# Kernel optimization log

Hardware: AMD Instinct MI355X
Metric: run time of the kernel (lower is better)

The kernel has to match this reference:

```python
import jax, jax.numpy as jnp
from jax import lax
import numpy as np

B, CIN, T, H, W = 32, 512, 16, 7, 7
A = 9                 # 3 scales x 3 ratios
STRIDE = 16.0
NMS_THRESH = 0.7      # cfg.TEST.RPN_NMS_THRESH
POST_NMS = 300        # cfg.TEST.RPN_POST_NMS_TOP_N


def _gen_anchors():
    # faithful port of generate_anchors(base_size=16, ratios=[0.5,1,2], scales=[4,8,16])
    base = 16.0
    ratios = np.array([0.5, 1.0, 2.0])
    scales = np.array([4.0, 8.0, 16.0])
    ctr = (base - 1.0) / 2.0
    size = base * base
    ws = np.round(np.sqrt(size / ratios))
    hs = np.round(ws * ratios)
    def mk(ws, hs, xc, yc):
        return np.stack([xc - 0.5 * (ws - 1), yc - 0.5 * (hs - 1),
                         xc + 0.5 * (ws - 1), yc + 0.5 * (hs - 1)], 1)
    ratio_anchors = mk(ws, hs, ctr, ctr)            # [3,4]
    outs = []
    for a in ratio_anchors:                         # scale enum per ratio anchor
        w = a[2] - a[0] + 1.0
        h = a[3] - a[1] + 1.0
        xc = a[0] + 0.5 * (w - 1)
        yc = a[1] + 0.5 * (h - 1)
        outs.append(mk(w * scales, h * scales, xc, yc))
    return np.concatenate(outs, 0).astype(np.float32)  # [9,4]


def _shifted_anchors():
    sx = (np.arange(W) * STRIDE).astype(np.float32)
    sy = (np.arange(H) * STRIDE).astype(np.float32)
    mx, my = np.meshgrid(sx, sy)                    # x fastest, matches HWA flatten
    shifts = np.stack([mx.ravel(), my.ravel(), mx.ravel(), my.ravel()], 1)  # [K,4]
    return (shifts[:, None, :] + _gen_anchors()[None, :, :]).reshape(-1, 4)  # [K*A,4]

_ALL_ANCHORS = jnp.asarray(_shifted_anchors())      # [441,4]


def conv3d(x, w, b, pad):
    y = lax.conv_general_dilated(x, w, (1, 1, 1),
                                 [(pad[0], pad[0]), (pad[1], pad[1]), (pad[2], pad[2])],
                                 dimension_numbers=('NCDHW', 'OIDHW', 'NCDHW'))
    return y + b[None, :, None, None, None]


def conv1x1(x, w, b):
    return jnp.einsum('bchw,oc->bohw', x, w[:, :, 0, 0]) + b[None, :, None, None]


def softmax_2way(score):
    # reshape(x,2) -> softmax over dim 1 -> reshape back (fg/bg pairwise softmax)
    b, c, h, w = score.shape
    s = score.reshape(b, 2, (c // 2) * h, w)
    return jax.nn.softmax(s, axis=1).reshape(b, c, h, w)


def bbox_decode(anchors, deltas):
    # anchors [N,4], deltas [B,N,4] -> boxes [B,N,4] (bbox_transform_inv)
    w = anchors[:, 2] - anchors[:, 0] + 1.0
    h = anchors[:, 3] - anchors[:, 1] + 1.0
    cx = anchors[:, 0] + 0.5 * w
    cy = anchors[:, 1] + 0.5 * h
    pcx = deltas[..., 0] * w + cx
    pcy = deltas[..., 1] * h + cy
    pw = jnp.exp(deltas[..., 2]) * w
    ph = jnp.exp(deltas[..., 3]) * h
    return jnp.stack([pcx - 0.5 * pw, pcy - 0.5 * ph,
                      pcx + 0.5 * pw, pcy + 0.5 * ph], axis=-1)


def clip_boxes(boxes, info):
    # boxes [N,4], info = (im_h, im_w, scale)
    x1 = jnp.clip(boxes[:, 0], 0.0, info[1] - 1.0)
    y1 = jnp.clip(boxes[:, 1], 0.0, info[0] - 1.0)
    x2 = jnp.clip(boxes[:, 2], 0.0, info[1] - 1.0)
    y2 = jnp.clip(boxes[:, 3], 0.0, info[0] - 1.0)
    return jnp.stack([x1, y1, x2, y2], 1)


def nms_single(boxes, scores):
    # greedy NMS, fixed shapes: boxes [N,4] -> kept boxes padded to [POST_NMS,4]
    order = jnp.argsort(-scores)
    b = boxes[order]
    n = b.shape[0]
    areas = (b[:, 2] - b[:, 0] + 1.0) * (b[:, 3] - b[:, 1] + 1.0)
    idx = jnp.arange(n)
    def body(i, keep):
        xx1 = jnp.maximum(b[i, 0], b[:, 0])
        yy1 = jnp.maximum(b[i, 1], b[:, 1])
        xx2 = jnp.minimum(b[i, 2], b[:, 2])
        yy2 = jnp.minimum(b[i, 3], b[:, 3])
        inter = jnp.clip(xx2 - xx1 + 1.0, 0.0) * jnp.clip(yy2 - yy1 + 1.0, 0.0)
        iou = inter / (areas[i] + areas - inter)
        sup = (idx > i) & (iou > NMS_THRESH) & keep[i]
        return keep & ~sup
    keep = lax.fori_loop(0, n, body, jnp.ones((n,), bool))
    sel = jnp.sort(jnp.where(keep, idx, n))[:POST_NMS]
    valid = sel < n
    selc = jnp.minimum(sel, n - 1)
    return jnp.where(valid[:, None], b[selc], 0.0)


def proposal_layer(cls_prob, bbox_pred, im_info):
    b = cls_prob.shape[0]
    scores = cls_prob[:, A:, :, :].transpose(0, 2, 3, 1).reshape(b, -1)   # fg scores [B,K*A]
    deltas = bbox_pred.transpose(0, 2, 3, 1).reshape(b, -1, 4)
    props = bbox_decode(_ALL_ANCHORS, deltas)
    props = jax.vmap(clip_boxes)(props, im_info)
    boxes = jax.vmap(nms_single)(props, scores)                           # [B,POST_NMS,4]
    bidx = jnp.broadcast_to(jnp.arange(b, dtype=boxes.dtype)[:, None, None],
                            (b, POST_NMS, 1))
    return jnp.concatenate([bidx, boxes], axis=2)                         # [B,POST_NMS,5]


def setup_inputs() -> dict:
    key = jax.random.key(0)
    ks = jax.random.split(key, 8)
    s = 0.05
    return {
        'base_feat': jax.random.normal(ks[0], (B, CIN, T, H, W), jnp.float32),
        'im_info': jnp.tile(jnp.array([[112.0, 112.0, 1.0]], jnp.float32), (B, 1)),
        'gt_boxes': jnp.zeros((B, 1, 7), jnp.float32),
        'num_boxes': jnp.zeros((B,), jnp.int32),
        'rpn_conv_w': jax.random.normal(ks[1], (512, CIN, 3, 3, 3), jnp.float32) * s,
        'rpn_conv_b': jnp.zeros((512,), jnp.float32),
        't16_w': jax.random.normal(ks[2], (512, 512, 16, 3, 3), jnp.float32) * s,
        't16_b': jnp.zeros((512,), jnp.float32),
        'cls_w': jax.random.normal(ks[3], (2 * A, 512, 1, 1), jnp.float32) * s,
        'cls_b': jnp.zeros((2 * A,), jnp.float32),
        'bbox_w': jax.random.normal(ks[4], (4 * A, 512, 1, 1), jnp.float32) * s,
        'bbox_b': jnp.zeros((4 * A,), jnp.float32),
    }


def reference(base_feat, im_info, gt_boxes, num_boxes,
              rpn_conv_w, rpn_conv_b, t16_w, t16_b,
              cls_w, cls_b, bbox_w, bbox_b):
    x = jax.nn.relu(conv3d(base_feat, rpn_conv_w, rpn_conv_b, (1, 1, 1)))     # [B,512,16,7,7]
    f16 = jax.nn.relu(conv3d(x, t16_w, t16_b, (0, 1, 1)))                     # [B,512,1,7,7]
    f16 = f16.transpose(0, 2, 1, 3, 4).reshape(-1, 512, H, W)                 # [B,512,7,7]
    cls_score = conv1x1(f16, cls_w, cls_b)                                    # [B,18,7,7]
    cls_prob = softmax_2way(cls_score)
    bbox_pred = conv1x1(f16, bbox_w, bbox_b)                                  # [B,36,7,7]
    # proposals use .data in the original -> detached
    rois = proposal_layer(lax.stop_gradient(cls_prob),
                          lax.stop_gradient(bbox_pred), im_info)
    return rois, cls_prob, bbox_pred
```

## Files before the change

kernel.cpp:

```cpp
#include <hip/hip_runtime.h>
#include <hip/hip_bf16.h>
#include <cmath>

typedef __bf16 bf16_t;
typedef unsigned short u16;
typedef unsigned int u32;
typedef float f32x4 __attribute__((ext_vector_type(4)));
typedef short s16x8 __attribute__((ext_vector_type(8)));
typedef u32   u32x4 __attribute__((ext_vector_type(4)));
#define DEVINL __device__ __forceinline__
#define POSTN 300

#define XPT_OFF  0ull
#define YT_OFF   23887872ull
#define F_OFF    45121536ull
#define PART_OFF 48332800ull
#define SC_OFF   51544064ull
#define BX_OFF   51600512ull
#define K1_OFF   51826304ull
#define K2_OFF   51881600ull
#define FLAG_OFF 52176512ull
#define NEED     52176516ull

DEVINL float ldf(const void* p, long i, int f32m) {
  return f32m ? ((const float*)p)[i] : (float)(((const bf16_t*)p)[i]);
}

DEVINL float clampf(float v, float lo, float hi) {
  if (!(v == v)) return lo;
  if (v < lo) return lo;
  if (v > hi) return hi;
  return v;
}

DEVINL u16 b16u(float v) {
  bf16_t h = (bf16_t)v;
  u16 r;
  __builtin_memcpy(&r, &h, 2);
  return r;
}

__global__ __launch_bounds__(256) void detect_dtype(const void* bf, const void* w1, int* flag) {
  __shared__ int cnt;
  int tid = threadIdx.x;
  if (tid == 0) cnt = 0;
  __syncthreads();
  float a = (float)(((const bf16_t*)bf)[2 * tid]);
  float b = (float)(((const bf16_t*)w1)[2 * tid]);
  int wc = 0;
  if (!(a == a) || fabsf(a) > 1e20f || (a != 0.f && fabsf(a) < 1e-20f)) wc++;
  if (!(b == b) || fabsf(b) > 1e20f || (b != 0.f && fabsf(b) < 1e-20f)) wc++;
  atomicAdd(&cnt, wc);
  __syncthreads();
  if (tid == 0) *flag = (cnt >= 16) ? 1 : 0;
}

__global__ __launch_bounds__(256) void build_koff(int* k1, int* k2) {
  int i = blockIdx.x * 256 + threadIdx.x;
  if (i < 13824) {
    int ci = i / 27, tap = i % 27;
    k1[i] = ci * 1458 + (tap / 9) * 81 + ((tap % 9) / 3) * 9 + (tap % 3);
  }
  if (i < 73728) {
    int ci = i / 144, tap = i % 144;
    k2[i] = ci * 1296 + (tap / 9) * 81 + ((tap % 9) / 3) * 9 + (tap % 3);
  }
}

__global__ __launch_bounds__(256) void pad_x(const void* __restrict__ X, float* __restrict__ XpT,
                                             const int* __restrict__ flagp, int cb) {
  int f32m = *flagp;
  long e = (long)blockIdx.x * 256 + threadIdx.x;
  if (e >= 8L * 512 * 784) return;
  int f = (int)(e % 784);
  long bc = e / 784;
  int t = f / 49, h = (f % 49) / 7, w = f % 7;
  float v = ldf(X, ((long)cb * 512 * 784) + bc * 784 + f, f32m);
  XpT[bc * 1458 + (t + 1) * 81 + (h + 1) * 9 + (w + 1)] = v;
}

template <int MODE>
__global__ __launch_bounds__(256) void gemm_f32(
    const float* __restrict__ Act, const void* __restrict__ Wgt, const void* __restrict__ bias,
    float* __restrict__ Yt, float* __restrict__ Part,
    const int* __restrict__ koff, const int* __restrict__ flagp) {
  const int f32m = *flagp;
  if (MODE == 1 && f32m == 0) return;
  const int tid = threadIdx.x;
  int mt, nt, s = 0;
  if (MODE == 1) { mt = blockIdx.x % 98; nt = blockIdx.x / 98; }
  else           { mt = blockIdx.x % 7;  nt = (blockIdx.x / 7) % 8; s = blockIdx.x / 56; }
  const int m0 = mt * 64, n0 = nt * 64;
  const int K     = (MODE == 1) ? 13824 : 18432;
  const int kBase = (MODE == 1) ? 0     : s * 18432;
  const int WROW  = (MODE == 1) ? 13824 : 73728;

  __shared__ __align__(16) float As[64][68];
  __shared__ __align__(16) float Bs[64][68];

  const int am = tid & 63, akq = tid >> 6;
  long aBase;
  {
    int m = m0 + am;
    if (MODE == 1) {
      int b = m / 784, r = m % 784, t = r / 49, h = (r % 49) / 7, w = r % 7;
      aBase = (long)b * (512 * 1458) + t * 81 + h * 9 + w;
    } else {
      if (m > 391) m = 391;
      int b = m / 49, r = m % 49, h = r / 7, w = r % 7;
      aBase = (long)b * (512 * 1296) + h * 9 + w;
    }
  }
  const int bn = tid >> 2, bks = (tid & 3) * 16;
  const long bBase = (long)(n0 + bn) * WROW + kBase;

  float acc[4][4] = {{0.f}};
  const int tx = tid & 15, ty = tid >> 4;

  for (int k0 = 0; k0 < K; k0 += 64) {
    __syncthreads();
#pragma unroll
    for (int j = 0; j < 16; j++) {
      int kk = akq * 16 + j;
      As[kk][am] = Act[aBase + koff[kBase + k0 + kk]];
    }
#pragma unroll
    for (int j = 0; j < 16; j++) {
      int kk = bks + j;
      Bs[kk][bn] = ldf(Wgt, bBase + k0 + kk, f32m);
    }
    __syncthreads();
#pragma unroll 8
    for (int k = 0; k < 64; k++) {
      f32x4 a = *(const f32x4*)&As[k][tx * 4];
      f32x4 b = *(const f32x4*)&Bs[k][ty * 4];
#pragma unroll
      for (int i = 0; i < 4; i++)
#pragma unroll
        for (int j = 0; j < 4; j++) acc[i][j] += a[i] * b[j];
    }
  }

#pragma unroll
  for (int i = 0; i < 4; i++) {
    int m = m0 + tx * 4 + i;
#pragma unroll
    for (int j = 0; j < 4; j++) {
      int n = n0 + ty * 4 + j;
      if (MODE == 1) {
        int b = m / 784, r = m % 784, t = r / 49, h = (r % 49) / 7, w = r % 7;
        float v = acc[i][j] + ldf(bias, n, f32m);
        v = fmaxf(v, 0.f);
        Yt[(long)(b * 512 + n) * 1296 + t * 81 + (h + 1) * 9 + (w + 1)] = v;
      } else {
        if (m < 392) Part[((long)s * 392 + m) * 512 + n] = acc[i][j];
      }
    }
  }
}

__global__ __launch_bounds__(256) void gemm_mf1(
    const float* __restrict__ Act, const void* __restrict__ Wgt, const void* __restrict__ bias,
    float* __restrict__ Yt, const int* __restrict__ koff, const int* __restrict__ flagp) {
  if (*flagp != 0) return;
  const int tid = threadIdx.x;
  const int mt = blockIdx.x % 49, nt = blockIdx.x / 49;
  const int m0 = mt * 128, n0 = nt * 64;

  __shared__ u16 As[128 * 64];
  __shared__ u16 Bs[64 * 64];

  const int am = tid & 127, khu = tid >> 7;
  long aBase;
  {
    int m = m0 + am;
    int b = m / 784, r = m % 784, t = r / 49, h = (r % 49) / 7, w = r % 7;
    aBase = (long)b * (512 * 1458) + t * 81 + h * 9 + w;
  }
  const float* __restrict__ Ap = Act + aBase;
  const int awb = am * 64, asw = (am & 7) << 3;

  const int bn = tid & 63, bq = tid >> 6;
  const u16* __restrict__ Bp = (const u16*)Wgt + (long)(n0 + bn) * 13824;
  const int bwb = bn * 64, bsw = (bn & 7) << 3;

  const int lane = tid & 63, wv = tid >> 6;
  const int wm = (wv & 1) * 64, wn = (wv >> 1) * 32;
  const int lr = lane & 15, lq = lane >> 4;

  f32x4 acc[4][2];
#pragma unroll
  for (int i = 0; i < 4; ++i)
#pragma unroll
    for (int j = 0; j < 2; ++j) acc[i][j] = f32x4{0.f, 0.f, 0.f, 0.f};

  for (int k0 = 0; k0 < 13824; k0 += 64) {
    __syncthreads();
#pragma unroll
    for (int j = 0; j < 4; ++j) {
      const int o = k0 + khu * 32 + j * 8;
      const u16 e0 = b16u(Ap[koff[o + 0]]), e1 = b16u(Ap[koff[o + 1]]);
      const u16 e2 = b16u(Ap[koff[o + 2]]), e3 = b16u(Ap[koff[o + 3]]);
      const u16 e4 = b16u(Ap[koff[o + 4]]), e5 = b16u(Ap[koff[o + 5]]);
      const u16 e6 = b16u(Ap[koff[o + 6]]), e7 = b16u(Ap[koff[o + 7]]);
      u32x4 V = { (u32)e0 | ((u32)e1 << 16), (u32)e2 | ((u32)e3 << 16),
                  (u32)e4 | ((u32)e5 << 16), (u32)e6 | ((u32)e7 << 16) };
      *(u32x4*)&As[awb + ((khu * 32 + j * 8) ^ asw)] = V;
    }
    {
      const u32x4* wp = (const u32x4*)(Bp + k0 + bq * 16);
      *(u32x4*)&Bs[bwb + ((bq * 16) ^ bsw)] = wp[0];
      *(u32x4*)&Bs[bwb + ((bq * 16 + 8) ^ bsw)] = wp[1];
    }
    __syncthreads();
#pragma unroll
    for (int kk = 0; kk < 64; kk += 32) {
      const int kf = kk + lq * 8;
      s16x8 a[4], b[2];
#pragma unroll
      for (int fm = 0; fm < 4; ++fm) {
        const int row = wm + fm * 16 + lr;
        a[fm] = *(const s16x8*)&As[row * 64 + (kf ^ ((lr & 7) << 3))];
      }
#pragma unroll
      for (int fn = 0; fn < 2; ++fn) {
        const int row = wn + fn * 16 + lr;
        b[fn] = *(const s16x8*)&Bs[row * 64 + (kf ^ ((lr & 7) << 3))];
      }
#pragma unroll
      for (int fm = 0; fm < 4; ++fm)
#pragma unroll
        for (int fn = 0; fn < 2; ++fn)
          acc[fm][fn] = __builtin_amdgcn_mfma_f32_16x16x32_bf16(a[fm], b[fn], acc[fm][fn], 0, 0, 0);
    }
  }

#pragma unroll
  for (int fn = 0; fn < 2; ++fn) {
    const int n = n0 + wn + fn * 16 + lr;
    const float bv = (float)(((const bf16_t*)bias)[n]);
#pragma unroll
    for (int fm = 0; fm < 4; ++fm)
#pragma unroll
      for (int r = 0; r < 4; ++r) {
        const int m = m0 + wm + fm * 16 + lq * 4 + r;
        int b = m / 784, rr = m % 784, t = rr / 49, hh = (rr % 49) / 7, ww = rr % 7;
        float v = fmaxf(acc[fm][fn][r] + bv, 0.f);
        Yt[(long)(b * 512 + n) * 1296 + t * 81 + (hh + 1) * 9 + (ww + 1)] = v;
      }
  }
}

__global__ __launch_bounds__(256) void reduce2(const float* __restrict__ Part,
                                               const void* __restrict__ bias,
                                               float* __restrict__ F,
                                               const int* __restrict__ flagp, int chunk) {
  int f32m = *flagp;
  int idx = blockIdx.x * 256 + threadIdx.x;
  if (idx >= 392 * 512) return;
  int m = idx >> 9, n = idx & 511;
  float v = 0.f;
  for (int s = 0; s < 4; s++) v += Part[((long)s * 392 + m) * 512 + n];
  v += ldf(bias, n, f32m);
  F[((long)chunk * 392 + m) * 512 + n] = fmaxf(v, 0.f);
}

__global__ __launch_bounds__(256) void heads(
    const float* __restrict__ F, const void* __restrict__ cls_w, const void* __restrict__ cls_b,
    const void* __restrict__ bbox_w, const void* __restrict__ bbox_b,
    const void* __restrict__ im_info, float* __restrict__ out_cls, float* __restrict__ out_bbox,
    float* __restrict__ scores, float* __restrict__ boxes, const int* __restrict__ flagp) {
  int f32m = *flagp;
  int m = blockIdx.x;
  int bg = m / 49, r2 = m % 49, h = r2 / 7, w = r2 % 7;
  __shared__ float Fr[512];
  __shared__ float partial[256];
  __shared__ float outv[54];
  int tid = threadIdx.x;
  Fr[tid] = F[(long)m * 512 + tid];
  Fr[tid + 256] = F[(long)m * 512 + tid + 256];
  __syncthreads();
  int o = tid & 63, ch = tid >> 6;
  float p = 0.f;
  if (o < 54) {
    const void* wp = (o < 18) ? cls_w : bbox_w;
    long wrow = (o < 18) ? (long)o * 512 : (long)(o - 18) * 512;
    int c0 = ch * 128;
    for (int c = c0; c < c0 + 128; c++) p += Fr[c] * ldf(wp, wrow + c, f32m);
  }
  partial[tid] = p;
  __syncthreads();
  if (tid < 54) {
    float v = partial[tid] + partial[tid + 64] + partial[tid + 128] + partial[tid + 192];
    v += (tid < 18) ? ldf(cls_b, tid, f32m) : ldf(bbox_b, tid - 18, f32m);
    outv[tid] = v;
  }
  __syncthreads();
  if (tid < 18) {
    int a = tid % 9;
    float s0 = outv[a], s1 = outv[a + 9];
    float mx = fmaxf(s0, s1);
    float e0 = expf(s0 - mx), e1 = expf(s1 - mx);
    float pr = ((tid < 9) ? e0 : e1) / (e0 + e1);
    if (!(pr == pr)) pr = 0.f;
    out_cls[(((long)(bg * 18 + tid)) * 7 + h) * 7 + w] = pr;
    if (tid >= 9) scores[bg * 441 + (h * 7 + w) * 9 + a] = pr;
  } else if (tid < 54) {
    float v = outv[tid];
    if (!(v == v)) v = 0.f;
    out_bbox[(((long)(bg * 36 + (tid - 18))) * 7 + h) * 7 + w] = v;
  } else if (tid < 63) {
    int a = tid - 54;
    int ridx = a / 3, sidx = a % 3;
    float ratio = (ridx == 0) ? 0.5f : ((ridx == 1) ? 1.f : 2.f);
    float scale = (sidx == 0) ? 4.f : ((sidx == 1) ? 8.f : 16.f);
    float ws0 = rintf(sqrtf(256.f / ratio));
    float hs0 = rintf(ws0 * ratio);
    float x1 = 7.5f - 0.5f * (ws0 - 1.f), y1 = 7.5f - 0.5f * (hs0 - 1.f);
    float x2 = 7.5f + 0.5f * (ws0 - 1.f), y2 = 7.5f + 0.5f * (hs0 - 1.f);
    float w_ = x2 - x1 + 1.f, h_ = y2 - y1 + 1.f;
    float xc = x1 + 0.5f * (w_ - 1.f), yc = y1 + 0.5f * (h_ - 1.f);
    float ws2 = w_ * scale, hs2 = h_ * scale;
    float ax1 = xc - 0.5f * (ws2 - 1.f) + w * 16.f;
    float ay1 = yc - 0.5f * (hs2 - 1.f) + h * 16.f;
    float ax2 = xc + 0.5f * (ws2 - 1.f) + w * 16.f;
    float ay2 = yc + 0.5f * (hs2 - 1.f) + h * 16.f;
    float wA = ax2 - ax1 + 1.f, hA = ay2 - ay1 + 1.f;
    float cxA = ax1 + 0.5f * wA, cyA = ay1 + 0.5f * hA;
    float d0 = outv[18 + 4 * a], d1 = outv[19 + 4 * a];
    float d2 = outv[20 + 4 * a], d3 = outv[21 + 4 * a];
    float pcx = d0 * wA + cxA, pcy = d1 * hA + cyA;
    float pw = expf(d2) * wA, ph = expf(d3) * hA;
    float iw = ldf(im_info, bg * 3 + 1, f32m) - 1.f;
    float ih = ldf(im_info, bg * 3 + 0, f32m) - 1.f;
    float bx1 = clampf(pcx - 0.5f * pw, 0.f, iw);
    float by1 = clampf(pcy - 0.5f * ph, 0.f, ih);
    float bx2 = clampf(pcx + 0.5f * pw, 0.f, iw);
    float by2 = clampf(pcy + 0.5f * ph, 0.f, ih);
    int ai = bg * 441 + (h * 7 + w) * 9 + a;
    boxes[ai * 4 + 0] = bx1; boxes[ai * 4 + 1] = by1;
    boxes[ai * 4 + 2] = bx2; boxes[ai * 4 + 3] = by2;
  }
}

__global__ __launch_bounds__(256) void nms_kernel(const float* __restrict__ scores,
                                                  const float* __restrict__ boxes,
                                                  float* __restrict__ rois) {
  int bg = blockIdx.x;
  int tid = threadIdx.x;
  __shared__ float rsc[441];
  __shared__ unsigned short ord[441];
  __shared__ float sbx[441][4];
  __shared__ float sar[441];
  __shared__ unsigned long long sup[441][8];
  __shared__ unsigned long long kw[8];
  for (int i = tid; i < 441; i += 256) { rsc[i] = scores[bg * 441 + i]; ord[i] = (unsigned short)i; }
  if (tid < 8) kw[tid] = 0ull;
  __syncthreads();
  for (int i = tid; i < 441; i += 256) {
    float si = rsc[i];
    int rk = 0;
    for (int j = 0; j < 441; j++) {
      float sj = rsc[j];
      rk += (sj > si) || (sj == si && j < i);
    }
    if (rk < 441) ord[rk] = (unsigned short)i;
  }
  __syncthreads();
  for (int r = tid; r < 441; r += 256) {
    int i = ord[r];
    float x1 = boxes[(bg * 441 + i) * 4 + 0], y1 = boxes[(bg * 441 + i) * 4 + 1];
    float x2 = boxes[(bg * 441 + i) * 4 + 2], y2 = boxes[(bg * 441 + i) * 4 + 3];
    sbx[r][0] = x1; sbx[r][1] = y1; sbx[r][2] = x2; sbx[r][3] = y2;
    sar[r] = (x2 - x1 + 1.f) * (y2 - y1 + 1.f);
  }
  __syncthreads();
  for (int task = tid; task < 441 * 7; task += 256) {
    int r = task / 7, wd = task % 7;
    float x1 = sbx[r][0], y1 = sbx[r][1], x2 = sbx[r][2], y2 = sbx[r][3];
    float ar = sar[r];
    unsigned long long msk = 0ull;
    int jbase = wd * 64;
    for (int bit = 0; bit < 64; bit++) {
      int j = jbase + bit;
      if (j > r && j < 441) {
        float xx1 = fmaxf(x1, sbx[j][0]);
        float yy1 = fmaxf(y1, sbx[j][1]);
        float xx2 = fminf(x2, sbx[j][2]);
        float yy2 = fminf(y2, sbx[j][3]);
        float iwv = fmaxf(xx2 - xx1 + 1.f, 0.f);
        float ihv = fmaxf(yy2 - yy1 + 1.f, 0.f);
        float inter = iwv * ihv;
        float iou = inter / (ar + sar[j] - inter);
        if (iou > 0.7f) msk |= (1ull << bit);
      }
    }
    sup[r][wd] = msk;
  }
  __syncthreads();
  if (tid < 64) {
    int wd = (tid < 7) ? tid : 7;
    unsigned long long rmw = 0ull;
    for (int i = 0; i < 441; i++) {
      int ow = i >> 6, obit = i & 63;
      int mykeep = ((rmw >> obit) & 1ull) ? 0 : 1;
      int kept = __shfl(mykeep, ow, 64);
      if (kept && wd < 7) rmw |= sup[i][wd];
    }
    if (wd < 7) {
      unsigned long long k = ~rmw;
      if (wd == 6) k &= (1ull << 57) - 1;
      kw[wd] = k;
    }
  }
  __syncthreads();
  for (int r = tid; r < POSTN; r += 256) {
    long oo = ((long)bg * POSTN + r) * 5;
    rois[oo] = (float)bg;
    rois[oo + 1] = 0.f; rois[oo + 2] = 0.f;
    rois[oo + 3] = 0.f; rois[oo + 4] = 0.f;
  }
  __syncthreads();
  for (int r = tid; r < 441; r += 256) {
    int wd = r >> 6, bit = r & 63;
    if ((kw[wd] >> bit) & 1ull) {
      int slot = 0;
      for (int q = 0; q < wd; q++) slot += __popcll(kw[q]);
      slot += __popcll(kw[wd] & ((1ull << bit) - 1ull));
      if (slot < POSTN) {
        long oo = ((long)bg * POSTN + slot) * 5;
        rois[oo + 1] = sbx[r][0];
        rois[oo + 2] = sbx[r][1];
        rois[oo + 3] = sbx[r][2];
        rois[oo + 4] = sbx[r][3];
      }
    }
  }
}

__global__ __launch_bounds__(256) void scrub_f32(float* __restrict__ o, int n) {
  int i = blockIdx.x * 256 + threadIdx.x;
  if (i >= n) return;
  float v = o[i];
  if (!(v == v) || fabsf(v) > 1e30f) o[i] = 0.f;
}

__global__ __launch_bounds__(256) void fallback_out(float* __restrict__ out, int total) {
  int i = blockIdx.x * 256 + threadIdx.x;
  if (i >= total) return;
  out[i] = 0.f;
}

extern "C" void kernel_launch(void* const* d_in, const int* in_sizes, int n_in,
                              void* d_out, int out_size, void* d_ws, size_t ws_size,
                              hipStream_t stream) {
  const void* base_feat = d_in[0];
  const void* im_info   = d_in[1];
  const void* w1 = d_in[4];
  const void* b1 = d_in[5];
  const void* w2 = d_in[6];
  const void* b2 = d_in[7];
  const void* cw = d_in[8];
  const void* cb = d_in[9];
  const void* bw = d_in[10];
  const void* bb = d_in[11];
  float* out = (float*)d_out;

  if (ws_size < NEED) {
    fallback_out<<<(out_size + 255) / 256, 256, 0, stream>>>(out, out_size);
    return;
  }

  char* ws = (char*)d_ws;
  float* XpT  = (float*)(ws + XPT_OFF);
  float* Yt   = (float*)(ws + YT_OFF);
  float* F    = (float*)(ws + F_OFF);
  float* Part = (float*)(ws + PART_OFF);
  float* Sc   = (float*)(ws + SC_OFF);
  float* Bx   = (float*)(ws + BX_OFF);
  int*   K1   = (int*)(ws + K1_OFF);
  int*   K2   = (int*)(ws + K2_OFF);
  int*   Flag = (int*)(ws + FLAG_OFF);

  detect_dtype<<<1, 256, 0, stream>>>(base_feat, w1, Flag);
  build_koff<<<288, 256, 0, stream>>>(K1, K2);

  for (int c = 0; c < 4; c++) {
    hipMemsetAsync(XpT, 0, 23887872ull, stream);
    hipMemsetAsync(Yt, 0, 21233664ull, stream);
    pad_x<<<12544, 256, 0, stream>>>(base_feat, XpT, Flag, c * 8);
    gemm_f32<1><<<784, 256, 0, stream>>>(XpT, w1, b1, Yt, nullptr, K1, Flag);
    gemm_mf1<<<392, 256, 0, stream>>>(XpT, w1, b1, Yt, K1, Flag);
    gemm_f32<2><<<224, 256, 0, stream>>>(Yt, w2, nullptr, nullptr, Part, K2, Flag);
    reduce2<<<784, 256, 0, stream>>>(Part, b2, F, Flag, c);
  }

  heads<<<1568, 256, 0, stream>>>(F, cw, cb, bw, bb, im_info,
                                  out + 48000, out + 76224, Sc, Bx, Flag);
  nms_kernel<<<32, 256, 0, stream>>>(Sc, Bx, out);
  scrub_f32<<<(out_size + 255) / 256, 256, 0, stream>>>(out, out_size);
}
```

Baseline: 12.65 ms.

## Run second conv on bf16 MFMA with three-way split activations

In the bf16 input path, the second 3D conv GEMM moves from the fp32 SIMT kernel to a new MFMA kernel. The first conv's output is stored as a three-term bf16 split (packed high/mid words plus a separate low word), so the bf16 product keeps near-fp32 accuracy. The padded input is also stored directly as bf16 instead of fp32, halving gather traffic for the first GEMM. The cost is three MFMAs per tile and extra split/pack work when storing and loading the intermediate.

Measured after the change: 10.35 ms. 1.22x faster.

```diff
diff --git a/kernel.cpp b/kernel.cpp
--- a/kernel.cpp
+++ b/kernel.cpp
@@ -12,6 +12,7 @@
 #define POSTN 300
 
 #define XPT_OFF  0ull
+#define YTL_OFF  11943936ull
 #define YT_OFF   23887872ull
 #define F_OFF    45121536ull
 #define PART_OFF 48332800ull
@@ -33,11 +34,15 @@
   return v;
 }
 
-DEVINL u16 b16u(float v) {
-  bf16_t h = (bf16_t)v;
-  u16 r;
-  __builtin_memcpy(&r, &h, 2);
-  return r;
+DEVINL void split3(float v, u16& hb, u16& mb, u16& lb) {
+  bf16_t h = (bf16_t)v; float fh = (float)h;
+  float r1 = v - fh;
+  bf16_t m = (bf16_t)r1; float fm_ = (float)m;
+  float r2 = r1 - fm_;
+  bf16_t l = (bf16_t)r2;
+  __builtin_memcpy(&hb, &h, 2);
+  __builtin_memcpy(&mb, &m, 2);
+  __builtin_memcpy(&lb, &l, 2);
 }
 
 __global__ __launch_bounds__(256) void detect_dtype(const void* bf, const void* w1, int* flag) {
@@ -67,7 +72,8 @@
   }
 }
 
-__global__ __launch_bounds__(256) void pad_x(const void* __restrict__ X, float* __restrict__ XpT,
+__global__ __launch_bounds__(256) void pad_x(const void* __restrict__ X,
+                                             float* __restrict__ XpT, u16* __restrict__ Xp16,
                                              const int* __restrict__ flagp, int cb) {
   int f32m = *flagp;
   long e = (long)blockIdx.x * 256 + threadIdx.x;
@@ -75,8 +81,10 @@
   int f = (int)(e % 784);
   long bc = e / 784;
   int t = f / 49, h = (f % 49) / 7, w = f % 7;
-  float v = ldf(X, ((long)cb * 512 * 784) + bc * 784 + f, f32m);
-  XpT[bc * 1458 + (t + 1) * 81 + (h + 1) * 9 + (w + 1)] = v;
+  long src = (long)cb * 512 * 784 + bc * 784 + f;
+  long idx = bc * 1458 + (t + 1) * 81 + (h + 1) * 9 + (w + 1);
+  if (f32m) XpT[idx] = ((const float*)X)[src];
+  else      Xp16[idx] = ((const u16*)X)[src];
 }
 
 template <int MODE>
@@ -85,7 +93,7 @@
     float* __restrict__ Yt, float* __restrict__ Part,
     const int* __restrict__ koff, const int* __restrict__ flagp) {
   const int f32m = *flagp;
-  if (MODE == 1 && f32m == 0) return;
+  if (f32m == 0) return;
   const int tid = threadIdx.x;
   int mt, nt, s = 0;
   if (MODE == 1) { mt = blockIdx.x % 98; nt = blockIdx.x / 98; }
@@ -160,8 +168,9 @@
 }
 
 __global__ __launch_bounds__(256) void gemm_mf1(
-    const float* __restrict__ Act, const void* __restrict__ Wgt, const void* __restrict__ bias,
-    float* __restrict__ Yt, const int* __restrict__ koff, const int* __restrict__ flagp) {
+    const u16* __restrict__ Act16, const void* __restrict__ Wgt, const void* __restrict__ bias,
+    u32* __restrict__ YtHM, u16* __restrict__ YtL,
+    const int* __restrict__ koff, const int* __restrict__ flagp) {
   if (*flagp != 0) return;
   const int tid = threadIdx.x;
   const int mt = blockIdx.x % 49, nt = blockIdx.x / 49;
@@ -177,7 +186,7 @@
     int b = m / 784, r = m % 784, t = r / 49, h = (r % 49) / 7, w = r % 7;
     aBase = (long)b * (512 * 1458) + t * 81 + h * 9 + w;
   }
-  const float* __restrict__ Ap = Act + aBase;
+  const u16* __restrict__ Ap = Act16 + aBase;
   const int awb = am * 64, asw = (am & 7) << 3;
 
   const int bn = tid & 63, bq = tid >> 6;
@@ -199,10 +208,10 @@
 #pragma unroll
     for (int j = 0; j < 4; ++j) {
       const int o = k0 + khu * 32 + j * 8;
-      const u16 e0 = b16u(Ap[koff[o + 0]]), e1 = b16u(Ap[koff[o + 1]]);
-      const u16 e2 = b16u(Ap[koff[o + 2]]), e3 = b16u(Ap[koff[o + 3]]);
-      const u16 e4 = b16u(Ap[koff[o + 4]]), e5 = b16u(Ap[koff[o + 5]]);
-      const u16 e6 = b16u(Ap[koff[o + 6]]), e7 = b16u(Ap[koff[o + 7]]);
+      const u16 e0 = Ap[koff[o + 0]], e1 = Ap[koff[o + 1]];
+      const u16 e2 = Ap[koff[o + 2]], e3 = Ap[koff[o + 3]];
+      const u16 e4 = Ap[koff[o + 4]], e5 = Ap[koff[o + 5]];
+      const u16 e6 = Ap[koff[o + 6]], e7 = Ap[koff[o + 7]];
       u32x4 V = { (u32)e0 | ((u32)e1 << 16), (u32)e2 | ((u32)e3 << 16),
                   (u32)e4 | ((u32)e5 << 16), (u32)e6 | ((u32)e7 << 16) };
       *(u32x4*)&As[awb + ((khu * 32 + j * 8) ^ asw)] = V;
@@ -246,7 +255,113 @@
         const int m = m0 + wm + fm * 16 + lq * 4 + r;
         int b = m / 784, rr = m % 784, t = rr / 49, hh = (rr % 49) / 7, ww = rr % 7;
         float v = fmaxf(acc[fm][fn][r] + bv, 0.f);
-        Yt[(long)(b * 512 + n) * 1296 + t * 81 + (hh + 1) * 9 + (ww + 1)] = v;
+        u16 hb, mb, lb; split3(v, hb, mb, lb);
+        long idx = (long)(b * 512 + n) * 1296 + t * 81 + (hh + 1) * 9 + (ww + 1);
+        YtHM[idx] = ((u32)hb << 16) | mb;
+        YtL[idx] = lb;
+      }
+  }
+}
+
+__global__ __launch_bounds__(256) void gemm_mf2(
+    const u32* __restrict__ AHM, const u16* __restrict__ AL, const void* __restrict__ Wgt,
+    float* __restrict__ Part, const int* __restrict__ koff, const int* __restrict__ flagp) {
+  if (*flagp != 0) return;
+  const int tid = threadIdx.x;
+  const int mt = blockIdx.x % 7, nt = (blockIdx.x / 7) % 8, s = blockIdx.x / 56;
+  const int m0 = mt * 64, n0 = nt * 64;
+  const int kBase = s * 18432;
+
+  __shared__ u16 AsH[64 * 64], AsM[64 * 64], AsL[64 * 64];
+  __shared__ u16 Bs[64 * 64];
+
+  const int am = tid & 63, kq = tid >> 6;
+  long aBase;
+  {
+    int m = m0 + am; if (m > 391) m = 391;
+    int b = m / 49, r = m % 49, h = r / 7, w = r % 7;
+    aBase = (long)b * (512 * 1296) + h * 9 + w;
+  }
+  const u32* __restrict__ ApHM = AHM + aBase;
+  const u16* __restrict__ ApL  = AL + aBase;
+  const int awb = am * 64, asw = (am & 7) << 3;
+
+  const int bn = tid & 63, bq = tid >> 6;
+  const u16* __restrict__ Bp = (const u16*)Wgt + (long)(n0 + bn) * 73728 + kBase;
+  const int bwb = bn * 64, bsw = (bn & 7) << 3;
+
+  const int lane = tid & 63, wv = tid >> 6;
+  const int wm = (wv & 1) * 32, wn = (wv >> 1) * 32;
+  const int lr = lane & 15, lq = lane >> 4;
+
+  f32x4 acc[2][2];
+#pragma unroll
+  for (int i = 0; i < 2; ++i)
+#pragma unroll
+    for (int j = 0; j < 2; ++j) acc[i][j] = f32x4{0.f, 0.f, 0.f, 0.f};
+
+  for (int k0 = 0; k0 < 18432; k0 += 64) {
+    __syncthreads();
+#pragma unroll
+    for (int g = 0; g < 2; ++g) {
+      const int o = kBase + k0 + kq * 16 + g * 8;
+      const int i0 = koff[o + 0], i1 = koff[o + 1], i2 = koff[o + 2], i3 = koff[o + 3],
+                i4 = koff[o + 4], i5 = koff[o + 5], i6 = koff[o + 6], i7 = koff[o + 7];
+      const u32 q0 = ApHM[i0], q1 = ApHM[i1], q2 = ApHM[i2], q3 = ApHM[i3],
+                q4 = ApHM[i4], q5 = ApHM[i5], q6 = ApHM[i6], q7 = ApHM[i7];
+      const int wi = awb + ((kq * 16 + g * 8) ^ asw);
+      u32x4 H = { (q0 >> 16) | (q1 & 0xffff0000u), (q2 >> 16) | (q3 & 0xffff0000u),
+                  (q4 >> 16) | (q5 & 0xffff0000u), (q6 >> 16) | (q7 & 0xffff0000u) };
+      *(u32x4*)&AsH[wi] = H;
+      u32x4 M = { (q0 & 0xffffu) | (q1 << 16), (q2 & 0xffffu) | (q3 << 16),
+                  (q4 & 0xffffu) | (q5 << 16), (q6 & 0xffffu) | (q7 << 16) };
+      *(u32x4*)&AsM[wi] = M;
+      u32x4 L = { (u32)ApL[i0] | ((u32)ApL[i1] << 16), (u32)ApL[i2] | ((u32)ApL[i3] << 16),
+                  (u32)ApL[i4] | ((u32)ApL[i5] << 16), (u32)ApL[i6] | ((u32)ApL[i7] << 16) };
+      *(u32x4*)&AsL[wi] = L;
+    }
+    {
+      const u32x4* wp = (const u32x4*)(Bp + k0 + bq * 16);
+      *(u32x4*)&Bs[bwb + ((bq * 16) ^ bsw)] = wp[0];
+      *(u32x4*)&Bs[bwb + ((bq * 16 + 8) ^ bsw)] = wp[1];
+    }
+    __syncthreads();
+#pragma unroll
+    for (int kk = 0; kk < 64; kk += 32) {
+      const int kf = kk + lq * 8;
+      s16x8 ah[2], am_[2], al[2], b[2];
+#pragma unroll
+      for (int fm = 0; fm < 2; ++fm) {
+        const int off = (wm + fm * 16 + lr) * 64 + (kf ^ ((lr & 7) << 3));
+        ah[fm] = *(const s16x8*)&AsH[off];
+        am_[fm] = *(const s16x8*)&AsM[off];
+        al[fm] = *(const s16x8*)&AsL[off];
+      }
+#pragma unroll
+      for (int fn = 0; fn < 2; ++fn) {
+        const int off = (wn + fn * 16 + lr) * 64 + (kf ^ ((lr & 7) << 3));
+        b[fn] = *(const s16x8*)&Bs[off];
+      }
+#pragma unroll
+      for (int fm = 0; fm < 2; ++fm)
+#pragma unroll
+        for (int fn = 0; fn < 2; ++fn) {
+          acc[fm][fn] = __builtin_amdgcn_mfma_f32_16x16x32_bf16(ah[fm], b[fn], acc[fm][fn], 0, 0, 0);
+          acc[fm][fn] = __builtin_amdgcn_mfma_f32_16x16x32_bf16(am_[fm], b[fn], acc[fm][fn], 0, 0, 0);
+          acc[fm][fn] = __builtin_amdgcn_mfma_f32_16x16x32_bf16(al[fm], b[fn], acc[fm][fn], 0, 0, 0);
+        }
+    }
+  }
+
+#pragma unroll
+  for (int fn = 0; fn < 2; ++fn) {
+    const int n = n0 + wn + fn * 16 + lr;
+#pragma unroll
+    for (int fm = 0; fm < 2; ++fm)
+#pragma unroll
+      for (int r = 0; r < 4; ++r) {
+        const int m = m0 + wm + fm * 16 + lq * 4 + r;
+        if (m < 392) Part[((long)s * 392 + m) * 512 + n] = acc[fm][fn][r];
       }
   }
 }
@@ -473,7 +588,10 @@
 
   char* ws = (char*)d_ws;
   float* XpT  = (float*)(ws + XPT_OFF);
+  u16*   Xp16 = (u16*)(ws + XPT_OFF);
+  u16*   YtL  = (u16*)(ws + YTL_OFF);
   float* Yt   = (float*)(ws + YT_OFF);
+  u32*   YtHM = (u32*)(ws + YT_OFF);
   float* F    = (float*)(ws + F_OFF);
   float* Part = (float*)(ws + PART_OFF);
   float* Sc   = (float*)(ws + SC_OFF);
@@ -488,10 +606,11 @@
   for (int c = 0; c < 4; c++) {
     hipMemsetAsync(XpT, 0, 23887872ull, stream);
     hipMemsetAsync(Yt, 0, 21233664ull, stream);
-    pad_x<<<12544, 256, 0, stream>>>(base_feat, XpT, Flag, c * 8);
+    pad_x<<<12544, 256, 0, stream>>>(base_feat, XpT, Xp16, Flag, c * 8);
     gemm_f32<1><<<784, 256, 0, stream>>>(XpT, w1, b1, Yt, nullptr, K1, Flag);
-    gemm_mf1<<<392, 256, 0, stream>>>(XpT, w1, b1, Yt, K1, Flag);
+    gemm_mf1<<<392, 256, 0, stream>>>(Xp16, w1, b1, YtHM, YtL, K1, Flag);
     gemm_f32<2><<<224, 256, 0, stream>>>(Yt, w2, nullptr, nullptr, Part, K2, Flag);
+    gemm_mf2<<<224, 256, 0, stream>>>(YtHM, YtL, w2, Part, K2, Flag);
     reduce2<<<784, 256, 0, stream>>>(Part, b2, F, Flag, c);
   }
 
```
